# Kernel optimization log

Measured on AMD Instinct MI355X. Metric: run time of the kernel, lower is better.

The kernel has to match this reference:

```python
import math
import jax, jax.numpy as jnp
import numpy as np

N_HEADS = 16
D_HEAD = 128
D_ROPE = 64  # d_head // 2
ROPE_SCALE = 40.0


def _rotate_half(x):
    x1, x2 = jnp.split(x, 2, axis=-1)
    return jnp.concatenate([-x2, x1], axis=-1)


def _apply_rotary(x, cos, sin):
    # rotate only the first cos.shape[-1] dims of the rope slice
    half = cos.shape[-1]
    x_rot, x_base = x[..., :half], x[..., half:]
    x_rot = x_rot * cos + _rotate_half(x_rot) * sin
    return jnp.concatenate([x_rot, x_base], axis=-1)


def _forward(x, W_dkv, W_dq, W_uk, W_uv, W_uq, W_kr, W_qr, W_out):
    B, S, H = x.shape
    c_kv = x @ W_dkv                                   # [B,S,cd]
    c_q = x @ W_dq                                     # [B,S,cd]
    q_c = c_q @ W_uq                                   # [B,S,up]
    k_c = c_kv @ W_uk                                  # [B,S,up]
    v = (c_kv @ W_uv).reshape(B, S, N_HEADS, D_HEAD)   # [B,S,h,d]
    k_r = (x @ W_kr).reshape(B, S, N_HEADS, D_ROPE)
    q_r = (q_c @ W_qr).reshape(B, S, N_HEADS, D_ROPE)

    # RoPE (partial: first d_rope//2 dims rotated, rest passthrough)
    half_dim = D_ROPE // 2
    inv_freq = 1.0 / (10000.0 ** (jnp.arange(0, half_dim, 2, dtype=jnp.float32) / half_dim))
    t = jnp.arange(S, dtype=jnp.float32) / ROPE_SCALE
    freqs = jnp.einsum('i,j->ij', t, inv_freq)         # [S, d_rope//4]
    rotation = jnp.concatenate([freqs, freqs], axis=-1)  # [S, d_rope//2]
    cos = jnp.cos(rotation)[None, :, None, :]
    sin = jnp.sin(rotation)[None, :, None, :]
    k_rope = _apply_rotary(k_r, cos, sin)
    q_rope = _apply_rotary(q_r, cos, sin)

    k = jnp.concatenate([k_c.reshape(B, S, N_HEADS, D_HEAD - D_ROPE), k_rope], axis=-1)
    q = jnp.concatenate([q_c.reshape(B, S, N_HEADS, D_HEAD - D_ROPE), q_rope], axis=-1)

    # NOTE: faithful to source: einsum takes (k, q) in that order, and the
    # softmax result is computed but UNUSED (AV uses raw scores). Replicated.
    scores = jnp.einsum('bihd,bjhd->bhij', k, q) / math.sqrt(D_HEAD)
    out = jnp.einsum('bhij,bjhd->bihd', scores, v)     # [B,S,h,d]
    output = out.reshape(B, S, N_HEADS * D_HEAD) @ W_out
    return output, c_kv, k_rope


def setup_inputs() -> dict:
    key = jax.random.key(0)
    ks = jax.random.split(key, 9)
    B, S, H, CD, UP = 2, 2048, 2048, 1024, 1024
    w = lambda k, shp: jax.random.normal(k, shp, dtype=jnp.float32) * 0.02
    return {
        'x': jax.random.normal(ks[0], (B, S, H), dtype=jnp.float32),
        'W_dkv': w(ks[1], (H, CD)),
        'W_dq': w(ks[2], (H, CD)),
        'W_uk': w(ks[3], (CD, UP)),
        'W_uv': w(ks[4], (CD, N_HEADS * D_HEAD)),
        'W_uq': w(ks[5], (CD, UP)),
        'W_kr': w(ks[6], (H, N_HEADS * D_ROPE)),
        'W_qr': w(ks[7], (CD, N_HEADS * D_ROPE)),
        'W_out': w(ks[8], (N_HEADS * D_HEAD, H)),
    }


def reference(x, W_dkv, W_dq, W_uk, W_uv, W_uq, W_kr, W_qr, W_out):
    return _forward(x, W_dkv, W_dq, W_uk, W_uv, W_uq, W_kr, W_qr, W_out)
```

## Files before the change

### kernel.cpp

```cpp
#include <hip/hip_runtime.h>
#include <math.h>

typedef _Float16 half8 __attribute__((ext_vector_type(8)));
typedef float floatx4 __attribute__((ext_vector_type(4)));

typedef const uint32_t __attribute__((address_space(1)))* gp1_t;
typedef uint32_t __attribute__((address_space(3)))* lp3_t;
#define GLDS16(g, l) __builtin_amdgcn_global_load_lds((gp1_t)(const void*)(g), (lp3_t)(void*)(l), 16, 0, 0)

#define BK 32

__global__ __launch_bounds__(256) void gemm_fast(
    const _Float16* __restrict__ A, const _Float16* __restrict__ B,
    float* __restrict__ Cf, _Float16* __restrict__ Ch,
    int Kc, long lda, long ldb, long ldcf, long ldch,
    int cmap, long cf_lo, long cf_hi, float alpha, int nh, int nsk,
    long aoff_b, long aoff_h, long boff_b, long boff_h,
    long coff_b, long coff_h, long coff_s)
{
    __shared__ __align__(16) _Float16 As[128 * BK];
    __shared__ __align__(16) _Float16 Bs[128 * BK];

    const int z = blockIdx.z;
    const int hs = nh * nsk;
    const int zb = z / hs;
    const int r0_ = z % hs;
    const int zh = r0_ / nsk;
    const int ks = r0_ % nsk;

    const _Float16* Ab = A + (long)zb * aoff_b + (long)zh * aoff_h + (long)ks * Kc;
    const _Float16* Bb = B + (long)zb * boff_b + (long)zh * boff_h + (long)ks * Kc;
    const long cofs = (long)zb * coff_b + (long)zh * coff_h + (long)ks * coff_s;

    const long m0 = (long)blockIdx.y * 128;
    const long n0 = (long)blockIdx.x * 128;
    const int t = threadIdx.x;
    const int wave = t >> 6, lane = t & 63;
    const int lr = lane & 15, lq = lane >> 4;
    const int wm = (wave & 1) * 64, wn = (wave >> 1) * 64;

    const int c0 = wave * 64 + lane;
    const int c1 = c0 + 256;
    const _Float16* ga0 = Ab + (m0 + (c0 >> 2)) * lda + (c0 & 3) * 8;
    const _Float16* ga1 = Ab + (m0 + (c1 >> 2)) * lda + (c1 & 3) * 8;
    const _Float16* gb0 = Bb + (n0 + (c0 >> 2)) * ldb + (c0 & 3) * 8;
    const _Float16* gb1 = Bb + (n0 + (c1 >> 2)) * ldb + (c1 & 3) * 8;
    _Float16* lA0 = As + wave * 512;
    _Float16* lA1 = As + 2048 + wave * 512;
    _Float16* lB0 = Bs + wave * 512;
    _Float16* lB1 = Bs + 2048 + wave * 512;

    floatx4 acc[4][4];
    #pragma unroll
    for (int i = 0; i < 4; ++i)
        #pragma unroll
        for (int j = 0; j < 4; ++j) acc[i][j] = (floatx4){0.f, 0.f, 0.f, 0.f};

    for (int k0 = 0; k0 < Kc; k0 += BK) {
        GLDS16(ga0, lA0); GLDS16(ga1, lA1);
        GLDS16(gb0, lB0); GLDS16(gb1, lB1);
        ga0 += BK; ga1 += BK; gb0 += BK; gb1 += BK;
        __syncthreads();

        half8 a[4], b[4];
        #pragma unroll
        for (int i = 0; i < 4; ++i) a[i] = *(const half8*)(As + (wm + i * 16 + lr) * BK + lq * 8);
        #pragma unroll
        for (int j = 0; j < 4; ++j) b[j] = *(const half8*)(Bs + (wn + j * 16 + lr) * BK + lq * 8);
        #pragma unroll
        for (int i = 0; i < 4; ++i)
            #pragma unroll
            for (int j = 0; j < 4; ++j)
                acc[i][j] = __builtin_amdgcn_mfma_f32_16x16x32_f16(a[i], b[j], acc[i][j], 0, 0, 0);
        __syncthreads();
    }

    #pragma unroll
    for (int i = 0; i < 4; ++i)
        #pragma unroll
        for (int j = 0; j < 4; ++j)
            #pragma unroll
            for (int r = 0; r < 4; ++r) {
                long row = m0 + wm + i * 16 + lq * 4 + r;
                long col = n0 + wn + j * 16 + lr;
                float v = alpha * acc[i][j][r];
                if (Ch) {
                    long cm = cmap ? ((col >> 6) * 128 + (col & 63)) : col;
                    Ch[cofs + row * ldch + cm] = (_Float16)v;
                }
                if (Cf && col >= cf_lo && col < cf_hi)
                    Cf[cofs + row * ldcf + (col - cf_lo)] = v;
            }
}

__global__ void cast_f16_kernel(const float* __restrict__ in, _Float16* __restrict__ out, int n)
{
    int i = blockIdx.x * 256 + threadIdx.x;
    if (i < n) out[i] = (_Float16)in[i];
}

__global__ void trx_kernel(const float* __restrict__ in0, const float* __restrict__ in1,
                           const float* __restrict__ in2,
                           _Float16* __restrict__ o0, _Float16* __restrict__ o1,
                           _Float16* __restrict__ o2, int R, int C)
{
    const float* in = blockIdx.z == 0 ? in0 : (blockIdx.z == 1 ? in1 : in2);
    _Float16* out = blockIdx.z == 0 ? o0 : (blockIdx.z == 1 ? o1 : o2);
    __shared__ float tbuf[32][33];
    int c0 = blockIdx.x * 32, r0 = blockIdx.y * 32;
    for (int i = threadIdx.y; i < 32; i += 8)
        tbuf[i][threadIdx.x] = in[(long)(r0 + i) * C + c0 + threadIdx.x];
    __syncthreads();
    for (int i = threadIdx.y; i < 32; i += 8)
        out[(long)(c0 + i) * R + r0 + threadIdx.x] = (_Float16)tbuf[threadIdx.x][i];
}

__global__ void rope_k_kernel(const _Float16* __restrict__ catA,
                              float* __restrict__ krope_out,
                              _Float16* __restrict__ k_flat)
{
    int idx = blockIdx.x * 256 + threadIdx.x;
    int bs = idx >> 10;
    int c = idx & 1023;
    int h = c >> 6, d = c & 63;
    long base = (long)bs * 3072 + 2048;
    float x = (float)catA[base + c];
    float y = x;
    if (d < 32) {
        int s = bs & 2047;
        int j = d & 15;
        float invf = powf(10000.0f, -(float)j / 16.0f);
        float ang = ((float)s / 40.0f) * invf;
        float other = (d < 16) ? -(float)catA[base + c + 16] : (float)catA[base + c - 16];
        y = x * cosf(ang) + other * sinf(ang);
    }
    krope_out[idx] = y;
    k_flat[(long)bs * 2048 + h * 128 + 64 + d] = (_Float16)y;
}

__global__ void rope_qT_kernel(const _Float16* __restrict__ q_crT,
                               _Float16* __restrict__ qT)
{
    long idx = (long)blockIdx.x * 256 + threadIdx.x;
    int row = (int)(idx >> 12);
    int col = (int)(idx & 4095);
    int h = row >> 7, d = row & 127;
    if (d < 64) {
        qT[idx] = q_crT[(long)(h * 64 + d) * 4096 + col];
    } else {
        int dd = d - 64;
        long base = (long)(1024 + h * 64) * 4096 + col;
        float x = (float)q_crT[base + (long)dd * 4096];
        float y = x;
        if (dd < 32) {
            int s = col & 2047;
            int j = dd & 15;
            float invf = powf(10000.0f, -(float)j / 16.0f);
            float ang = ((float)s / 40.0f) * invf;
            float other = (dd < 16) ? -(float)q_crT[base + (long)(dd + 16) * 4096]
                                    :  (float)q_crT[base + (long)(dd - 16) * 4096];
            y = x * cosf(ang) + other * sinf(ang);
        }
        qT[idx] = (_Float16)y;
    }
}

__global__ void reduce8_cast_kernel(const float* __restrict__ in, _Float16* __restrict__ out)
{
    int i = blockIdx.x * 256 + threadIdx.x;
    float s = 0.f;
    #pragma unroll
    for (int j = 0; j < 8; ++j) s += in[i + j * 524288];
    out[i] = (_Float16)s;
}

extern "C" void kernel_launch(void* const* d_in, const int* in_sizes, int n_in,
                              void* d_out, int out_size, void* d_ws, size_t ws_size,
                              hipStream_t stream)
{
    const float* x     = (const float*)d_in[0];
    const float* W_dkv = (const float*)d_in[1];
    const float* W_dq  = (const float*)d_in[2];
    const float* W_uk  = (const float*)d_in[3];
    const float* W_uv  = (const float*)d_in[4];
    const float* W_uq  = (const float*)d_in[5];
    const float* W_kr  = (const float*)d_in[6];
    const float* W_qr  = (const float*)d_in[7];
    const float* W_out = (const float*)d_in[8];

    float* out_main  = (float*)d_out;
    float* out_ckv   = out_main + 8388608;
    float* out_krope = out_ckv + 4194304;

    char* w = (char*)d_ws;
    size_t off = 0;
    auto alloc = [&](size_t bytes) { void* p = w + off; off += (bytes + 255) & ~(size_t)255; return p; };

    _Float16* catA    = (_Float16*)alloc(25165824);
    _Float16* WcatT   = (_Float16*)alloc(12582912);
    _Float16* WukT    = (_Float16*)alloc(2097152);
    _Float16* WuqcatT = (_Float16*)alloc(4194304);
    _Float16* WqrT    = (_Float16*)alloc(2097152);
    _Float16* Wuqh    = (_Float16*)alloc(2097152);
    _Float16* WuvT    = (_Float16*)alloc(4194304);
    _Float16* WoutT   = (_Float16*)alloc(8388608);
    void* reg_xq      = alloc(16777216);
    _Float16* k_flat  = (_Float16*)alloc(16777216);
    _Float16* vT      = (_Float16*)alloc(16777216);
    void* reg_qp      = alloc(16777216);

    _Float16* xh     = (_Float16*)reg_xq;
    _Float16* qT     = (_Float16*)reg_xq;
    _Float16* q_crT  = (_Float16*)reg_qp;
    float*    Mbuf32p = (float*)reg_qp;
    _Float16* PT     = (_Float16*)reg_qp;
    _Float16* WuqT   = WuqcatT;
    _Float16* WuqrT  = WuqcatT + 1048576;
    _Float16* Mbuf16 = WukT;

    #define GF(A_,B_,Cf_,Ch_,M_,N_,Kc_,lda_,ldb_,ldcf_,ldch_,cmap_,cflo_,cfhi_,alpha_,nb_,nh_,nsk_,ab,ah,bb,bh,cb,ch2,cs) \
        hipLaunchKernelGGL(gemm_fast, dim3((N_)/128,(M_)/128,(nb_)*(nh_)*(nsk_)), dim3(256), 0, stream, \
            A_, B_, Cf_, Ch_, (int)(Kc_), (long)(lda_), (long)(ldb_), (long)(ldcf_), (long)(ldch_), \
            cmap_, (long)(cflo_), (long)(cfhi_), (float)(alpha_), nh_, nsk_, \
            (long)(ab),(long)(ah),(long)(bb),(long)(bh),(long)(cb),(long)(ch2),(long)(cs))

    hipLaunchKernelGGL(cast_f16_kernel, dim3(32768), dim3(256), 0, stream, x, xh, 8388608);
    hipLaunchKernelGGL(cast_f16_kernel, dim3(4096), dim3(256), 0, stream, W_uq, Wuqh, 1048576);
    hipLaunchKernelGGL(trx_kernel, dim3(32, 64, 3), dim3(32, 8), 0, stream,
        W_dkv, W_dq, W_kr, WcatT, WcatT + 2097152, WcatT + 4194304, 2048, 1024);
    hipLaunchKernelGGL(trx_kernel, dim3(32, 32, 3), dim3(32, 8), 0, stream,
        W_uk, W_uq, W_qr, WukT, WuqT, WqrT, 1024, 1024);
    hipLaunchKernelGGL(trx_kernel, dim3(64, 32, 1), dim3(32, 8), 0, stream,
        W_uv, W_uv, W_uv, WuvT, WuvT, WuvT, 1024, 2048);
    hipLaunchKernelGGL(trx_kernel, dim3(64, 64, 1), dim3(32, 8), 0, stream,
        W_out, W_out, W_out, WoutT, WoutT, WoutT, 2048, 2048);

    GF(xh, WcatT, out_ckv, catA, 4096, 3072, 2048, 2048, 2048, 1024, 3072, 0, 0, 1024, 1.0,
       1, 1, 1, 0,0,0,0,0,0,0);
    GF(WqrT, Wuqh, (float*)nullptr, WuqrT, 1024, 1024, 1024, 1024, 1024, 0, 1024, 0, 0, 0, 1.0,
       1, 1, 1, 0,0,0,0,0,0,0);
    GF(catA, WukT, (float*)nullptr, k_flat, 4096, 1024, 1024, 3072, 1024, 0, 2048, 1, 0, 0, 1.0,
       1, 1, 1, 0,0,0,0,0,0,0);
    GF(WuvT, catA, (float*)nullptr, vT, 2048, 4096, 1024, 1024, 3072, 0, 4096, 0, 0, 0, 1.0,
       1, 1, 1, 0,0,0,0,0,0,0);
    GF(WuqcatT, catA + 1024, (float*)nullptr, q_crT, 2048, 4096, 1024, 1024, 3072, 0, 4096, 0, 0, 0, 1.0,
       1, 1, 1, 0,0,0,0,0,0,0);
    hipLaunchKernelGGL(rope_k_kernel, dim3(16384), dim3(256), 0, stream, catA, out_krope, k_flat);
    hipLaunchKernelGGL(rope_qT_kernel, dim3(32768), dim3(256), 0, stream, q_crT, qT);
    GF(qT, vT, Mbuf32p, (_Float16*)nullptr, 128, 128, 256, 4096, 4096, 128, 0, 0, 0, 128,
       0.08838834764831845, 2, 16, 8, 2048, 524288, 2048, 524288, 262144, 16384, 524288);
    hipLaunchKernelGGL(reduce8_cast_kernel, dim3(2048), dim3(256), 0, stream, Mbuf32p, Mbuf16);
    GF(WoutT, Mbuf16, (float*)nullptr, PT, 2048, 128, 128, 2048, 128, 0, 2048, 0, 0, 0, 1.0,
       2, 16, 1, 0, 128, 262144, 16384, 4194304, 128, 0);
    GF(k_flat, PT, out_main, (_Float16*)nullptr, 2048, 2048, 2048, 2048, 2048, 2048, 0, 0, 0, 2048, 1.0,
       2, 1, 1, 4194304, 0, 4194304, 0, 4194304, 0, 0);

    #undef GF
}
```

Before: 504.2 us.

## Fuse RoPE into GEMM epilogues, merge prep kernels, batch V/Q up-projection GEMMs

Adds epilogue modes to the GEMM so that RoPE for k and q is applied directly when the projection results are written. This removes the separate rope_k and rope_qT kernels and their extra passes over intermediate buffers. The weight transposes and fp16 casts are merged into one prep kernel, which cuts launch overhead. The V and Q up-projections now run as a single batched launch with z-dimension 2, writing qT directly in per-head layout. The cost is more complex epilogues with scattered, less coalesced stores and transcendental math inside the GEMM.

```diff
diff --git a/kernel.cpp b/kernel.cpp
--- a/kernel.cpp
+++ b/kernel.cpp
@@ -13,8 +13,9 @@
 __global__ __launch_bounds__(256) void gemm_fast(
     const _Float16* __restrict__ A, const _Float16* __restrict__ B,
     float* __restrict__ Cf, _Float16* __restrict__ Ch,
+    float* __restrict__ Cx, _Float16* __restrict__ Cy,
     int Kc, long lda, long ldb, long ldcf, long ldch,
-    int cmap, long cf_lo, long cf_hi, float alpha, int nh, int nsk,
+    int cmap, long cf_lo, long cf_hi, float alpha, int nh, int nsk, int epi_mode,
     long aoff_b, long aoff_h, long boff_b, long boff_h,
     long coff_b, long coff_h, long coff_s)
 {
@@ -24,9 +25,9 @@
     const int z = blockIdx.z;
     const int hs = nh * nsk;
     const int zb = z / hs;
-    const int r0_ = z % hs;
-    const int zh = r0_ / nsk;
-    const int ks = r0_ % nsk;
+    const int rr = z % hs;
+    const int zh = rr / nsk;
+    const int ks = rr % nsk;
 
     const _Float16* Ab = A + (long)zb * aoff_b + (long)zh * aoff_h + (long)ks * Kc;
     const _Float16* Bb = B + (long)zb * boff_b + (long)zh * boff_h + (long)ks * Kc;
@@ -75,94 +76,163 @@
         __syncthreads();
     }
 
-    #pragma unroll
-    for (int i = 0; i < 4; ++i)
-        #pragma unroll
-        for (int j = 0; j < 4; ++j)
-            #pragma unroll
-            for (int r = 0; r < 4; ++r) {
-                long row = m0 + wm + i * 16 + lq * 4 + r;
-                long col = n0 + wn + j * 16 + lr;
-                float v = alpha * acc[i][j][r];
-                if (Ch) {
-                    long cm = cmap ? ((col >> 6) * 128 + (col & 63)) : col;
-                    Ch[cofs + row * ldch + cm] = (_Float16)v;
+    if (epi_mode == 0) {
+        #pragma unroll
+        for (int i = 0; i < 4; ++i)
+            #pragma unroll
+            for (int j = 0; j < 4; ++j)
+                #pragma unroll
+                for (int r = 0; r < 4; ++r) {
+                    long row = m0 + wm + i * 16 + lq * 4 + r;
+                    long col = n0 + wn + j * 16 + lr;
+                    float v = alpha * acc[i][j][r];
+                    if (Ch) {
+                        long cm = cmap ? ((col >> 6) * 128 + (col & 63)) : col;
+                        Ch[cofs + row * ldch + cm] = (_Float16)v;
+                    }
+                    if (Cf && col >= cf_lo && col < cf_hi)
+                        Cf[cofs + row * ldcf + (col - cf_lo)] = v;
                 }
-                if (Cf && col >= cf_lo && col < cf_hi)
-                    Cf[cofs + row * ldcf + (col - cf_lo)] = v;
+    } else if (epi_mode == 1) {
+        const int nb = (int)n0 + wn;
+        if (nb < 2048) {
+            #pragma unroll
+            for (int i = 0; i < 4; ++i)
+                #pragma unroll
+                for (int j = 0; j < 4; ++j)
+                    #pragma unroll
+                    for (int r = 0; r < 4; ++r) {
+                        long row = m0 + wm + i * 16 + lq * 4 + r;
+                        long col = n0 + wn + j * 16 + lr;
+                        float v = acc[i][j][r];
+                        Ch[row * 2048 + col] = (_Float16)v;
+                        if (nb < 1024) Cf[row * 1024 + col] = v;
+                    }
+        } else {
+            const int h = (nb - 2048) >> 6;
+            const float invf = powf(10000.0f, -(float)lr / 16.0f);
+            #pragma unroll
+            for (int i = 0; i < 4; ++i)
+                #pragma unroll
+                for (int r = 0; r < 4; ++r) {
+                    long row = m0 + wm + i * 16 + lq * 4 + r;
+                    int s = (int)row & 2047;
+                    float ang = ((float)s / 40.0f) * invf;
+                    float cv = cosf(ang), sv = sinf(ang);
+                    float v0 = acc[i][0][r], v1 = acc[i][1][r];
+                    float y[4] = { v0 * cv - v1 * sv, v1 * cv + v0 * sv,
+                                   acc[i][2][r], acc[i][3][r] };
+                    #pragma unroll
+                    for (int j = 0; j < 4; ++j) {
+                        int d = j * 16 + lr;
+                        Cx[row * 1024 + h * 64 + d] = y[j];
+                        Cy[row * 2048 + h * 128 + 64 + d] = (_Float16)y[j];
+                    }
+                }
+        }
+    } else {
+        if (zb == 0) {
+            #pragma unroll
+            for (int i = 0; i < 4; ++i)
+                #pragma unroll
+                for (int j = 0; j < 4; ++j)
+                    #pragma unroll
+                    for (int r = 0; r < 4; ++r) {
+                        long row = m0 + wm + i * 16 + lq * 4 + r;
+                        long col = n0 + wn + j * 16 + lr;
+                        Ch[cofs + row * ldch + col] = (_Float16)acc[i][j][r];
+                    }
+        } else {
+            const int mb = (int)m0 + wm;
+            if (mb < 1024) {
+                #pragma unroll
+                for (int i = 0; i < 4; ++i)
+                    #pragma unroll
+                    for (int j = 0; j < 4; ++j)
+                        #pragma unroll
+                        for (int r = 0; r < 4; ++r) {
+                            long u = m0 + wm + i * 16 + lq * 4 + r;
+                            long col = n0 + wn + j * 16 + lr;
+                            long qrow = ((u >> 6) << 7) + (u & 63);
+                            Ch[cofs + qrow * 4096 + col] = (_Float16)acc[i][j][r];
+                        }
+            } else {
+                const int h = (mb - 1024) >> 6;
+                const float invf = powf(10000.0f, -(float)(lq * 4) / 16.0f);
+                #pragma unroll
+                for (int j = 0; j < 4; ++j)
+                    #pragma unroll
+                    for (int r = 0; r < 4; ++r) {
+                        long col = n0 + wn + j * 16 + lr;
+                        int s = (int)col & 2047;
+                        int j16 = lq * 4 + r;
+                        float ivf = powf(10000.0f, -(float)j16 / 16.0f);
+                        float ang = ((float)s / 40.0f) * ivf;
+                        float cv = cosf(ang), sv = sinf(ang);
+                        float v0 = acc[0][j][r], v1 = acc[1][j][r];
+                        float y[4] = { v0 * cv - v1 * sv, v1 * cv + v0 * sv,
+                                       acc[2][j][r], acc[3][j][r] };
+                        #pragma unroll
+                        for (int i = 0; i < 4; ++i) {
+                            int dd = i * 16 + lq * 4 + r;
+                            long qrow = h * 128 + 64 + dd;
+                            Ch[cofs + qrow * 4096 + col] = (_Float16)y[i];
+                        }
+                    }
+                (void)invf;
             }
-}
-
-__global__ void cast_f16_kernel(const float* __restrict__ in, _Float16* __restrict__ out, int n)
-{
-    int i = blockIdx.x * 256 + threadIdx.x;
-    if (i < n) out[i] = (_Float16)in[i];
-}
-
-__global__ void trx_kernel(const float* __restrict__ in0, const float* __restrict__ in1,
-                           const float* __restrict__ in2,
-                           _Float16* __restrict__ o0, _Float16* __restrict__ o1,
-                           _Float16* __restrict__ o2, int R, int C)
-{
-    const float* in = blockIdx.z == 0 ? in0 : (blockIdx.z == 1 ? in1 : in2);
-    _Float16* out = blockIdx.z == 0 ? o0 : (blockIdx.z == 1 ? o1 : o2);
-    __shared__ float tbuf[32][33];
-    int c0 = blockIdx.x * 32, r0 = blockIdx.y * 32;
-    for (int i = threadIdx.y; i < 32; i += 8)
-        tbuf[i][threadIdx.x] = in[(long)(r0 + i) * C + c0 + threadIdx.x];
+        }
+    }
+}
+
+__device__ inline void tr_tile(const float* __restrict__ in, _Float16* __restrict__ out,
+                               int R, int C, int tile, int tx, int ty, float (*tb)[33])
+{
+    int tc = tile % (C >> 5), tr = tile / (C >> 5);
+    int c0 = tc * 32, r0 = tr * 32;
+    for (int i = ty; i < 32; i += 8)
+        tb[i][tx] = in[(long)(r0 + i) * C + c0 + tx];
     __syncthreads();
-    for (int i = threadIdx.y; i < 32; i += 8)
-        out[(long)(c0 + i) * R + r0 + threadIdx.x] = (_Float16)tbuf[threadIdx.x][i];
-}
-
-__global__ void rope_k_kernel(const _Float16* __restrict__ catA,
-                              float* __restrict__ krope_out,
-                              _Float16* __restrict__ k_flat)
-{
-    int idx = blockIdx.x * 256 + threadIdx.x;
-    int bs = idx >> 10;
-    int c = idx & 1023;
-    int h = c >> 6, d = c & 63;
-    long base = (long)bs * 3072 + 2048;
-    float x = (float)catA[base + c];
-    float y = x;
-    if (d < 32) {
-        int s = bs & 2047;
-        int j = d & 15;
-        float invf = powf(10000.0f, -(float)j / 16.0f);
-        float ang = ((float)s / 40.0f) * invf;
-        float other = (d < 16) ? -(float)catA[base + c + 16] : (float)catA[base + c - 16];
-        y = x * cosf(ang) + other * sinf(ang);
-    }
-    krope_out[idx] = y;
-    k_flat[(long)bs * 2048 + h * 128 + 64 + d] = (_Float16)y;
-}
-
-__global__ void rope_qT_kernel(const _Float16* __restrict__ q_crT,
-                               _Float16* __restrict__ qT)
-{
-    long idx = (long)blockIdx.x * 256 + threadIdx.x;
-    int row = (int)(idx >> 12);
-    int col = (int)(idx & 4095);
-    int h = row >> 7, d = row & 127;
-    if (d < 64) {
-        qT[idx] = q_crT[(long)(h * 64 + d) * 4096 + col];
-    } else {
-        int dd = d - 64;
-        long base = (long)(1024 + h * 64) * 4096 + col;
-        float x = (float)q_crT[base + (long)dd * 4096];
-        float y = x;
-        if (dd < 32) {
-            int s = col & 2047;
-            int j = dd & 15;
-            float invf = powf(10000.0f, -(float)j / 16.0f);
-            float ang = ((float)s / 40.0f) * invf;
-            float other = (dd < 16) ? -(float)q_crT[base + (long)(dd + 16) * 4096]
-                                    :  (float)q_crT[base + (long)(dd - 16) * 4096];
-            y = x * cosf(ang) + other * sinf(ang);
-        }
-        qT[idx] = (_Float16)y;
-    }
+    for (int i = ty; i < 32; i += 8)
+        out[(long)(c0 + i) * R + r0 + tx] = (_Float16)tb[tx][i];
+}
+
+__device__ inline void cast_blk(const float* __restrict__ in, _Float16* __restrict__ out,
+                                int blk, int tid)
+{
+    long idx = (long)blk * 2048 + tid * 8;
+    float4 a = ((const float4*)(in + idx))[0];
+    float4 b = ((const float4*)(in + idx))[1];
+    half8 h = { (_Float16)a.x, (_Float16)a.y, (_Float16)a.z, (_Float16)a.w,
+                (_Float16)b.x, (_Float16)b.y, (_Float16)b.z, (_Float16)b.w };
+    *(half8*)(out + idx) = h;
+}
+
+__global__ void prep_kernel(
+    const float* __restrict__ x, const float* __restrict__ W_dkv,
+    const float* __restrict__ W_dq, const float* __restrict__ W_uk,
+    const float* __restrict__ W_uv, const float* __restrict__ W_uq,
+    const float* __restrict__ W_kr, const float* __restrict__ W_qr,
+    const float* __restrict__ W_out,
+    _Float16* __restrict__ WcatT, _Float16* __restrict__ WukT,
+    _Float16* __restrict__ WuvT, _Float16* __restrict__ WuqcatT,
+    _Float16* __restrict__ WqrT, _Float16* __restrict__ Wuqh,
+    _Float16* __restrict__ WoutT, _Float16* __restrict__ xh)
+{
+    __shared__ float tb[32][33];
+    int blk = blockIdx.x;
+    int tid = threadIdx.x;
+    int tx = tid & 31, ty = tid >> 5;
+    if (blk < 2048)        tr_tile(W_dkv, WcatT,            2048, 1024, blk,         tx, ty, tb);
+    else if (blk < 4096)   tr_tile(W_dq,  WcatT + 2097152,  2048, 1024, blk - 2048,  tx, ty, tb);
+    else if (blk < 6144)   tr_tile(W_kr,  WcatT + 4194304,  2048, 1024, blk - 4096,  tx, ty, tb);
+    else if (blk < 7168)   tr_tile(W_uk,  WukT,             1024, 1024, blk - 6144,  tx, ty, tb);
+    else if (blk < 8192)   tr_tile(W_uq,  WuqcatT,          1024, 1024, blk - 7168,  tx, ty, tb);
+    else if (blk < 9216)   tr_tile(W_qr,  WqrT,             1024, 1024, blk - 8192,  tx, ty, tb);
+    else if (blk < 11264)  tr_tile(W_uv,  WuvT,             1024, 2048, blk - 9216,  tx, ty, tb);
+    else if (blk < 15360)  tr_tile(W_out, WoutT,            2048, 2048, blk - 11264, tx, ty, tb);
+    else if (blk < 19456)  cast_blk(x,    xh,   blk - 15360, tid);
+    else                   cast_blk(W_uq, Wuqh, blk - 19456, tid);
 }
 
 __global__ void reduce8_cast_kernel(const float* __restrict__ in, _Float16* __restrict__ out)
@@ -196,64 +266,54 @@
     size_t off = 0;
     auto alloc = [&](size_t bytes) { void* p = w + off; off += (bytes + 255) & ~(size_t)255; return p; };
 
-    _Float16* catA    = (_Float16*)alloc(25165824);
+    _Float16* catA    = (_Float16*)alloc(16777216);
     _Float16* WcatT   = (_Float16*)alloc(12582912);
     _Float16* WukT    = (_Float16*)alloc(2097152);
+    _Float16* WuvT    = (_Float16*)alloc(4194304);
     _Float16* WuqcatT = (_Float16*)alloc(4194304);
     _Float16* WqrT    = (_Float16*)alloc(2097152);
     _Float16* Wuqh    = (_Float16*)alloc(2097152);
-    _Float16* WuvT    = (_Float16*)alloc(4194304);
     _Float16* WoutT   = (_Float16*)alloc(8388608);
-    void* reg_xq      = alloc(16777216);
+    void*     reg_xm  = alloc(16777216);
     _Float16* k_flat  = (_Float16*)alloc(16777216);
     _Float16* vT      = (_Float16*)alloc(16777216);
-    void* reg_qp      = alloc(16777216);
-
-    _Float16* xh     = (_Float16*)reg_xq;
-    _Float16* qT     = (_Float16*)reg_xq;
-    _Float16* q_crT  = (_Float16*)reg_qp;
-    float*    Mbuf32p = (float*)reg_qp;
-    _Float16* PT     = (_Float16*)reg_qp;
-    _Float16* WuqT   = WuqcatT;
-    _Float16* WuqrT  = WuqcatT + 1048576;
-    _Float16* Mbuf16 = WukT;
-
-    #define GF(A_,B_,Cf_,Ch_,M_,N_,Kc_,lda_,ldb_,ldcf_,ldch_,cmap_,cflo_,cfhi_,alpha_,nb_,nh_,nsk_,ab,ah,bb,bh,cb,ch2,cs) \
+    _Float16* qT      = (_Float16*)alloc(16777216);
+
+    _Float16* xh      = (_Float16*)reg_xm;
+    float*    Mbuf32p = (float*)reg_xm;
+    _Float16* PT      = catA;
+    _Float16* WuqrT   = WuqcatT + 1048576;
+    _Float16* Mbuf16  = WukT;
+
+    #define GF(A_,B_,Cf_,Ch_,Cx_,Cy_,M_,N_,Kc_,lda_,ldb_,ldcf_,ldch_,cmap_,cflo_,cfhi_,alpha_,nb_,nh_,nsk_,mode_,ab,ah,bb,bh,cb,ch2,cs) \
         hipLaunchKernelGGL(gemm_fast, dim3((N_)/128,(M_)/128,(nb_)*(nh_)*(nsk_)), dim3(256), 0, stream, \
-            A_, B_, Cf_, Ch_, (int)(Kc_), (long)(lda_), (long)(ldb_), (long)(ldcf_), (long)(ldch_), \
-            cmap_, (long)(cflo_), (long)(cfhi_), (float)(alpha_), nh_, nsk_, \
+            A_, B_, Cf_, Ch_, Cx_, Cy_, (int)(Kc_), (long)(lda_), (long)(ldb_), (long)(ldcf_), (long)(ldch_), \
+            cmap_, (long)(cflo_), (long)(cfhi_), (float)(alpha_), nh_, nsk_, mode_, \
             (long)(ab),(long)(ah),(long)(bb),(long)(bh),(long)(cb),(long)(ch2),(long)(cs))
 
-    hipLaunchKernelGGL(cast_f16_kernel, dim3(32768), dim3(256), 0, stream, x, xh, 8388608);
-    hipLaunchKernelGGL(cast_f16_kernel, dim3(4096), dim3(256), 0, stream, W_uq, Wuqh, 1048576);
-    hipLaunchKernelGGL(trx_kernel, dim3(32, 64, 3), dim3(32, 8), 0, stream,
-        W_dkv, W_dq, W_kr, WcatT, WcatT + 2097152, WcatT + 4194304, 2048, 1024);
-    hipLaunchKernelGGL(trx_kernel, dim3(32, 32, 3), dim3(32, 8), 0, stream,
-        W_uk, W_uq, W_qr, WukT, WuqT, WqrT, 1024, 1024);
-    hipLaunchKernelGGL(trx_kernel, dim3(64, 32, 1), dim3(32, 8), 0, stream,
-        W_uv, W_uv, W_uv, WuvT, WuvT, WuvT, 1024, 2048);
-    hipLaunchKernelGGL(trx_kernel, dim3(64, 64, 1), dim3(32, 8), 0, stream,
-        W_out, W_out, W_out, WoutT, WoutT, WoutT, 2048, 2048);
-
-    GF(xh, WcatT, out_ckv, catA, 4096, 3072, 2048, 2048, 2048, 1024, 3072, 0, 0, 1024, 1.0,
-       1, 1, 1, 0,0,0,0,0,0,0);
-    GF(WqrT, Wuqh, (float*)nullptr, WuqrT, 1024, 1024, 1024, 1024, 1024, 0, 1024, 0, 0, 0, 1.0,
-       1, 1, 1, 0,0,0,0,0,0,0);
-    GF(catA, WukT, (float*)nullptr, k_flat, 4096, 1024, 1024, 3072, 1024, 0, 2048, 1, 0, 0, 1.0,
-       1, 1, 1, 0,0,0,0,0,0,0);
-    GF(WuvT, catA, (float*)nullptr, vT, 2048, 4096, 1024, 1024, 3072, 0, 4096, 0, 0, 0, 1.0,
-       1, 1, 1, 0,0,0,0,0,0,0);
-    GF(WuqcatT, catA + 1024, (float*)nullptr, q_crT, 2048, 4096, 1024, 1024, 3072, 0, 4096, 0, 0, 0, 1.0,
-       1, 1, 1, 0,0,0,0,0,0,0);
-    hipLaunchKernelGGL(rope_k_kernel, dim3(16384), dim3(256), 0, stream, catA, out_krope, k_flat);
-    hipLaunchKernelGGL(rope_qT_kernel, dim3(32768), dim3(256), 0, stream, q_crT, qT);
-    GF(qT, vT, Mbuf32p, (_Float16*)nullptr, 128, 128, 256, 4096, 4096, 128, 0, 0, 0, 128,
-       0.08838834764831845, 2, 16, 8, 2048, 524288, 2048, 524288, 262144, 16384, 524288);
+    hipLaunchKernelGGL(prep_kernel, dim3(19968), dim3(256), 0, stream,
+        x, W_dkv, W_dq, W_uk, W_uv, W_uq, W_kr, W_qr, W_out,
+        WcatT, WukT, WuvT, WuqcatT, WqrT, Wuqh, WoutT, xh);
+
+    GF(xh, WcatT, out_ckv, catA, out_krope, k_flat, 4096, 3072, 2048, 2048, 2048, 0, 0,
+       0, 0, 0, 1.0, 1, 1, 1, 1, 0,0,0,0,0,0,0);
+    GF(WqrT, Wuqh, (float*)nullptr, WuqrT, (float*)nullptr, (_Float16*)nullptr,
+       1024, 1024, 1024, 1024, 1024, 0, 1024, 0, 0, 0, 1.0, 1, 1, 1, 0, 0,0,0,0,0,0,0);
+    GF(catA, WukT, (float*)nullptr, k_flat, (float*)nullptr, (_Float16*)nullptr,
+       4096, 1024, 1024, 2048, 1024, 0, 2048, 1, 0, 0, 1.0, 1, 1, 1, 0, 0,0,0,0,0,0,0);
+    GF(WuvT, catA, (float*)nullptr, vT, (float*)nullptr, (_Float16*)nullptr,
+       2048, 4096, 1024, 1024, 2048, 0, 4096, 0, 0, 0, 1.0, 2, 1, 1, 2,
+       2097152, 0, 1024, 0, 8388608, 0, 0);
+    GF(qT, vT, Mbuf32p, (_Float16*)nullptr, (float*)nullptr, (_Float16*)nullptr,
+       128, 128, 256, 4096, 4096, 128, 0, 0, 0, 128, 0.08838834764831845, 2, 16, 8, 0,
+       2048, 524288, 2048, 524288, 262144, 16384, 524288);
     hipLaunchKernelGGL(reduce8_cast_kernel, dim3(2048), dim3(256), 0, stream, Mbuf32p, Mbuf16);
-    GF(WoutT, Mbuf16, (float*)nullptr, PT, 2048, 128, 128, 2048, 128, 0, 2048, 0, 0, 0, 1.0,
-       2, 16, 1, 0, 128, 262144, 16384, 4194304, 128, 0);
-    GF(k_flat, PT, out_main, (_Float16*)nullptr, 2048, 2048, 2048, 2048, 2048, 2048, 0, 0, 0, 2048, 1.0,
-       2, 1, 1, 4194304, 0, 4194304, 0, 4194304, 0, 0);
+    GF(WoutT, Mbuf16, (float*)nullptr, PT, (float*)nullptr, (_Float16*)nullptr,
+       2048, 128, 128, 2048, 128, 0, 2048, 0, 0, 0, 1.0, 2, 16, 1, 0,
+       0, 128, 262144, 16384, 4194304, 128, 0);
+    GF(k_flat, PT, out_main, (_Float16*)nullptr, (float*)nullptr, (_Float16*)nullptr,
+       2048, 2048, 2048, 2048, 2048, 2048, 0, 0, 0, 2048, 1.0, 2, 1, 1, 0,
+       4194304, 0, 4194304, 0, 4194304, 0, 0);
 
     #undef GF
 }
```

Result: faster. 474.8 us (-5.8%).
